# Kernel tuning notes

Measured on AMD Instinct MI355X. Metric: run time of the kernel, lower is better.

Reference implementation:

```python
import jax, jax.numpy as jnp
import numpy as np
import math

STRIDES = [8, 16, 32, 64, 128]
NUM_CLASSES = 80
NUM_ANCHORS = 9
_RATIOS = np.array([0.5, 1.0, 2.0])
_SCALES = 2.0 ** np.array([0.0, 1.0 / 3.0, 2.0 / 3.0])


def _base_anchors(base_size):
    # standard RetinaNet base anchors: 3 ratios x 3 scales, centered at origin
    a = np.zeros((9, 4))
    a[:, 2:] = base_size * np.tile(_SCALES, (2, 3)).T
    areas = a[:, 2] * a[:, 3]
    a[:, 2] = np.sqrt(areas / np.repeat(_RATIOS, 3))
    a[:, 3] = a[:, 2] * np.repeat(_RATIOS, 3)
    a[:, 0::2] -= np.tile(a[:, 2] * 0.5, (2, 1)).T
    a[:, 1::2] -= np.tile(a[:, 3] * 0.5, (2, 1)).T
    return a


def _make_anchors(featmap_sizes):
    per_level = []
    for (h, w), s in zip(featmap_sizes, STRIDES):
        base = _base_anchors(4 * s)  # base_size = 4 * stride (RetinaNet convention)
        sx = (np.arange(w) + 0.5) * s
        sy = (np.arange(h) + 0.5) * s
        X, Y = np.meshgrid(sx, sy)
        shifts = np.stack([X.ravel(), Y.ravel(), X.ravel(), Y.ravel()], axis=1)
        # anchors vary fastest per location -> matches [B,H,W,A,*] flatten order
        per_level.append((shifts[:, None, :] + base[None, :, :]).reshape(-1, 4))
    return jnp.asarray(np.concatenate(per_level, axis=0), dtype=jnp.float32)


def _conv3x3(x, w, b):
    y = jax.lax.conv_general_dilated(x, w, (1, 1), 'SAME', dimension_numbers=('NCHW', 'OIHW', 'NCHW'))
    return y + b[None, :, None, None]


def _tower(x, ws, bs):
    for i in range(4):
        x = jax.nn.relu(_conv3x3(x, ws[i], bs[i]))
    return _conv3x3(x, ws[4], bs[4])


def _bbox_transform(anchors, deltas):
    # BBoxTransform with mean 0, std (0.1, 0.1, 0.2, 0.2)
    w = anchors[:, 2] - anchors[:, 0]
    h = anchors[:, 3] - anchors[:, 1]
    cx = anchors[:, 0] + 0.5 * w
    cy = anchors[:, 1] + 0.5 * h
    pcx = cx + deltas[..., 0] * 0.1 * w
    pcy = cy + deltas[..., 1] * 0.1 * h
    pw = jnp.exp(deltas[..., 2] * 0.2) * w
    ph = jnp.exp(deltas[..., 3] * 0.2) * h
    return jnp.stack([pcx - 0.5 * pw, pcy - 0.5 * ph, pcx + 0.5 * pw, pcy + 0.5 * ph], axis=-1)


def _heads(feats, cls_ws, cls_bs, reg_ws, reg_bs):
    B = feats[0].shape[0]
    cls_l, reg_l = [], []
    for f in feats:
        c = _tower(f, cls_ws, cls_bs)  # [B, 9*80, H, W]
        cls_l.append(jnp.transpose(c, (0, 2, 3, 1)).reshape(B, -1, NUM_CLASSES))
        r = _tower(f, reg_ws, reg_bs)  # [B, 9*4, H, W]
        reg_l.append(jnp.transpose(r, (0, 2, 3, 1)).reshape(B, -1, 4))
    return jnp.concatenate(cls_l, axis=1), jnp.concatenate(reg_l, axis=1)


def setup_inputs():
    key = jax.random.key(0)
    ks = jax.random.split(key, 32)
    B, C = 8, 256
    sizes = [(64, 64), (32, 32), (16, 16), (8, 8), (4, 4)]
    inp = {}
    for i, (h, w) in enumerate(sizes):
        inp['feat%d' % i] = jax.random.normal(ks[i], (B, C, h, w), dtype=jnp.float32)
    prior_bias = -math.log((1.0 - 0.01) / 0.01)

    def mk(k, out_ch, in_ch):
        std = math.sqrt(2.0 / (9.0 * out_ch))  # matches torch init normal_(0, sqrt(2/n))
        return jax.random.normal(k, (out_ch, in_ch, 3, 3), dtype=jnp.float32) * std

    ki = 5
    for i in range(4):
        inp['cls_w%d' % i] = mk(ks[ki], 256, 256); ki += 1
        inp['cls_b%d' % i] = jnp.zeros((256,), jnp.float32)
    inp['cls_w4'] = mk(ks[ki], NUM_ANCHORS * NUM_CLASSES, 256); ki += 1
    inp['cls_b4'] = jnp.full((NUM_ANCHORS * NUM_CLASSES,), prior_bias, jnp.float32)
    for i in range(4):
        inp['reg_w%d' % i] = mk(ks[ki], 256, 256); ki += 1
        inp['reg_b%d' % i] = jnp.zeros((256,), jnp.float32)
    inp['reg_w4'] = mk(ks[ki], NUM_ANCHORS * 4, 256); ki += 1
    inp['reg_b4'] = jnp.full((NUM_ANCHORS * 4,), prior_bias, jnp.float32)
    return inp


def reference(feat0, feat1, feat2, feat3, feat4,
              cls_w0, cls_b0, cls_w1, cls_b1, cls_w2, cls_b2, cls_w3, cls_b3, cls_w4, cls_b4,
              reg_w0, reg_b0, reg_w1, reg_b1, reg_w2, reg_b2, reg_w3, reg_b3, reg_w4, reg_b4):
    feats = [feat0, feat1, feat2, feat3, feat4]
    cls_ws = [cls_w0, cls_w1, cls_w2, cls_w3, cls_w4]
    cls_bs = [cls_b0, cls_b1, cls_b2, cls_b3, cls_b4]
    reg_ws = [reg_w0, reg_w1, reg_w2, reg_w3, reg_w4]
    reg_bs = [reg_b0, reg_b1, reg_b2, reg_b3, reg_b4]
    pred_cls, pred_reg = _heads(feats, cls_ws, cls_bs, reg_ws, reg_bs)
    anchors = _make_anchors([f.shape[-2:] for f in feats])  # [A, 4]
    boxes = _bbox_transform(anchors, pred_reg)  # [B, A, 4]
    probs = jax.nn.sigmoid(pred_cls)  # [B, A, 80]
    scores = jnp.max(probs, axis=2)
    class_id = jnp.argmax(probs, axis=2)
    return scores, class_id, boxes
```

## Files before the change

kernel.cpp:

```cpp
#include <hip/hip_runtime.h>
#include <math.h>

#define CIN 256
#define TLW 16
#define TLH 8
#define LIS 22

template<typename TI, typename TA, int CH, bool RELU>
__global__ __launch_bounds__(256, 2) void conv_tile(
    const TI* __restrict__ in, const float* __restrict__ wgt,
    const float* __restrict__ bias, TA* __restrict__ out,
    int H, int W, int C_out)
{
    const int NCH = CIN / CH;
    const int tilesX = (W + TLW - 1) / TLW;
    const int tx = (blockIdx.x % tilesX) * TLW;
    const int ty = (blockIdx.x / tilesX) * TLH;
    const int b  = blockIdx.y;
    const int co0 = blockIdx.z * 64;
    const int tid = threadIdx.x;
    const int tco = (tid >> 5) * 8;
    const int tpx = tid & 31;
    const int prow = tpx >> 2;
    const int pcol = (tpx & 3) * 4;

    __shared__ __align__(16) TA lw[CH * 9 * 64];
    __shared__ __align__(16) TA li[CH * 10 * LIS];

    TA acc[8][4];
    #pragma unroll
    for (int c = 0; c < 8; ++c)
        #pragma unroll
        for (int j = 0; j < 4; ++j) acc[c][j] = (TA)0;

    const int coLim = min(64, C_out - co0);

    for (int ch = 0; ch < NCH; ++ch) {
        const int ci0 = ch * CH;
        for (int idx = tid; idx < CH * 9 * 64; idx += 256) {
            int r  = idx >> 6;
            int co = idx & 63;
            TA v = (TA)0;
            if (co < coLim)
                v = (TA)wgt[(size_t)(co0 + co) * (CIN * 9) + (size_t)ci0 * 9 + r];
            lw[idx] = v;
        }
        for (int idx = tid; idx < CH * 10 * LIS; idx += 256) {
            int ci = idx / (10 * LIS);
            int rr = idx % (10 * LIS);
            int row = rr / LIS, col = rr % LIS;
            TA v = (TA)0;
            int iy = ty + row - 1, ix = tx + col - 1;
            if (col < TLW + 2 && iy >= 0 && iy < H && ix >= 0 && ix < W)
                v = (TA)in[(((size_t)b * CIN + ci0 + ci) * H + iy) * W + ix];
            li[idx] = v;
        }
        __syncthreads();
        #pragma unroll
        for (int ci = 0; ci < CH; ++ci) {
            #pragma unroll
            for (int ky = 0; ky < 3; ++ky) {
                const TA* ip = &li[ci * 10 * LIS + (prow + ky) * LIS + pcol];
                TA ir[6];
                #pragma unroll
                for (int t = 0; t < 6; ++t) ir[t] = ip[t];
                #pragma unroll
                for (int kx = 0; kx < 3; ++kx) {
                    const TA* wp = &lw[(ci * 9 + ky * 3 + kx) * 64 + tco];
                    TA wv[8];
                    #pragma unroll
                    for (int c = 0; c < 8; ++c) wv[c] = wp[c];
                    TA x0 = ir[kx], x1 = ir[kx + 1], x2 = ir[kx + 2], x3 = ir[kx + 3];
                    #pragma unroll
                    for (int c = 0; c < 8; ++c) {
                        acc[c][0] += wv[c] * x0;
                        acc[c][1] += wv[c] * x1;
                        acc[c][2] += wv[c] * x2;
                        acc[c][3] += wv[c] * x3;
                    }
                }
            }
        }
        __syncthreads();
    }

    const int oy = ty + prow;
    if (oy < H) {
        #pragma unroll
        for (int c = 0; c < 8; ++c) {
            int co = co0 + tco + c;
            if (co < C_out) {
                TA bv = (TA)bias[co];
                #pragma unroll
                for (int j = 0; j < 4; ++j) {
                    int ox = tx + pcol + j;
                    if (ox < W) {
                        TA v = acc[c][j] + bv;
                        if (RELU) v = v > (TA)0 ? v : (TA)0;
                        out[(((size_t)b * C_out + co) * H + oy) * W + ox] = v;
                    }
                }
            }
        }
    }
}

#define CH5 8
__global__ __launch_bounds__(256, 2) void conv_cls5(
    const double* __restrict__ in, const float* __restrict__ wgt,
    const float* __restrict__ bias, float* __restrict__ scores,
    float* __restrict__ cls_id,
    int H, int W, int level_off, int A_total, int b0)
{
    const int tilesX = (W + TLW - 1) / TLW;
    const int tx = (blockIdx.x % tilesX) * TLW;
    const int ty = (blockIdx.x / tilesX) * TLH;
    const int b  = blockIdx.y;
    const int a  = blockIdx.z;
    const int co0 = a * 80;
    const int tid = threadIdx.x;
    const int cog = tid >> 5;
    const int tco = cog * 10;
    const int tpx = tid & 31;
    const int prow = tpx >> 2;
    const int pcol = (tpx & 3) * 4;

    __shared__ __align__(16) double lw[CH5 * 9 * 80];
    __shared__ __align__(16) double li[CH5 * 10 * LIS];

    double acc[10][4];
    #pragma unroll
    for (int c = 0; c < 10; ++c)
        #pragma unroll
        for (int j = 0; j < 4; ++j) acc[c][j] = 0.0;

    for (int ch = 0; ch < CIN / CH5; ++ch) {
        const int ci0 = ch * CH5;
        for (int idx = tid; idx < CH5 * 9 * 80; idx += 256) {
            int r  = idx / 80;
            int co = idx % 80;
            lw[idx] = (double)wgt[(size_t)(co0 + co) * (CIN * 9)
                                  + (size_t)ci0 * 9 + r];
        }
        for (int idx = tid; idx < CH5 * 10 * LIS; idx += 256) {
            int ci = idx / (10 * LIS);
            int rr = idx % (10 * LIS);
            int row = rr / LIS, col = rr % LIS;
            double v = 0.0;
            int iy = ty + row - 1, ix = tx + col - 1;
            if (col < TLW + 2 && iy >= 0 && iy < H && ix >= 0 && ix < W)
                v = in[(((size_t)b * CIN + ci0 + ci) * H + iy) * W + ix];
            li[idx] = v;
        }
        __syncthreads();
        #pragma unroll
        for (int ci = 0; ci < CH5; ++ci) {
            #pragma unroll
            for (int ky = 0; ky < 3; ++ky) {
                const double* ip = &li[ci * 10 * LIS + (prow + ky) * LIS + pcol];
                double ir[6];
                #pragma unroll
                for (int t = 0; t < 6; ++t) ir[t] = ip[t];
                #pragma unroll
                for (int kx = 0; kx < 3; ++kx) {
                    const double* wp = &lw[(ci * 9 + ky * 3 + kx) * 80 + tco];
                    double wv[10];
                    #pragma unroll
                    for (int c = 0; c < 10; ++c) wv[c] = wp[c];
                    double x0 = ir[kx], x1 = ir[kx + 1], x2 = ir[kx + 2], x3 = ir[kx + 3];
                    #pragma unroll
                    for (int c = 0; c < 10; ++c) {
                        acc[c][0] += wv[c] * x0;
                        acc[c][1] += wv[c] * x1;
                        acc[c][2] += wv[c] * x2;
                        acc[c][3] += wv[c] * x3;
                    }
                }
            }
        }
        __syncthreads();
    }

    double* redM = lw;
    int*    redA = (int*)li;

    #pragma unroll
    for (int j = 0; j < 4; ++j) {
        double m = acc[0][j] + (double)bias[co0 + tco];
        int am = tco;
        #pragma unroll
        for (int c = 1; c < 10; ++c) {
            double v = acc[c][j] + (double)bias[co0 + tco + c];
            if (v > m) { m = v; am = tco + c; }
        }
        int p = prow * 16 + pcol + j;
        redM[p * 8 + cog] = m;
        redA[p * 8 + cog] = am;
    }
    __syncthreads();
    if (tid < 128) {
        int p = tid;
        double m = redM[p * 8]; int am = redA[p * 8];
        #pragma unroll
        for (int t = 1; t < 8; ++t)
            if (redM[p * 8 + t] > m) { m = redM[p * 8 + t]; am = redA[p * 8 + t]; }
        int oy = ty + (p >> 4), ox = tx + (p & 15);
        if (oy < H && ox < W) {
            size_t oi = (size_t)(b0 + b) * A_total + level_off
                      + (size_t)(oy * W + ox) * 9 + a;
            scores[oi] = (float)(1.0 / (1.0 + exp(-m)));
            cls_id[oi] = (float)am;
        }
    }
}

__global__ void boxes_ep(const float* __restrict__ reg5, float* __restrict__ boxes,
                         int H, int W, int level_off, int A_total, float stride,
                         int b0, int Bc)
{
    int idx = blockIdx.x * 256 + threadIdx.x;
    int total = Bc * H * W * 9;
    if (idx >= total) return;
    int a = idx % 9; int rest = idx / 9;
    int x = rest % W; rest /= W;
    int y = rest % H; int b = rest / H;

    float base = 4.f * stride;
    float scale = exp2f((float)(a % 3) * (1.f / 3.f));
    int ri = a / 3;
    float sr = (ri == 0) ? 0.70710678118654752f : (ri == 1 ? 1.f : 1.41421356237309505f);
    float wa = base * scale / sr;
    float ha = base * scale * sr;
    float cx = (x + 0.5f) * stride, cy = (y + 0.5f) * stride;

    size_t cs = (size_t)H * W;
    const float* rp = reg5 + (((size_t)b * 36 + a * 4) * H + y) * W + x;
    float d0 = rp[0], d1 = rp[cs], d2 = rp[2 * cs], d3 = rp[3 * cs];

    float pcx = cx + d0 * 0.1f * wa;
    float pcy = cy + d1 * 0.1f * ha;
    float pw  = expf(d2 * 0.2f) * wa;
    float ph  = expf(d3 * 0.2f) * ha;

    size_t oi = ((size_t)(b0 + b) * A_total + level_off
               + (size_t)(y * W + x) * 9 + a) * 4;
    boxes[oi + 0] = pcx - 0.5f * pw;
    boxes[oi + 1] = pcy - 0.5f * ph;
    boxes[oi + 2] = pcx + 0.5f * pw;
    boxes[oi + 3] = pcy + 0.5f * ph;
}

extern "C" void kernel_launch(void* const* d_in, const int* in_sizes, int n_in,
                              void* d_out, int out_size, void* d_ws, size_t ws_size,
                              hipStream_t stream)
{
    const float* feats[5];
    for (int i = 0; i < 5; ++i) feats[i] = (const float*)d_in[i];
    const float* cw[5]; const float* cb[5];
    const float* rw[5]; const float* rb[5];
    for (int i = 0; i < 5; ++i) {
        cw[i] = (const float*)d_in[5 + 2 * i];
        cb[i] = (const float*)d_in[6 + 2 * i];
        rw[i] = (const float*)d_in[15 + 2 * i];
        rb[i] = (const float*)d_in[16 + 2 * i];
    }

    const int A_total = 49104;
    float* scores = (float*)d_out;
    float* cls_id = scores + (size_t)8 * A_total;
    float* boxes  = scores + (size_t)2 * 8 * A_total;

    const int   Hs[5]      = {64, 32, 16, 8, 4};
    const float strides[5] = {8.f, 16.f, 32.f, 64.f, 128.f};
    const int   offs[5]    = {0, 36864, 46080, 48384, 48960};

    for (int l = 0; l < 5; ++l) {
        int H = Hs[l], W = Hs[l];
        size_t perb = (size_t)CIN * H * W;
        int Bc = 8;
        while (Bc > 1 && 2ull * Bc * perb * sizeof(double) > ws_size) Bc >>= 1;
        double* D0 = (double*)d_ws;
        double* D1 = D0 + (size_t)Bc * perb;
        int tiles = ((W + TLW - 1) / TLW) * ((H + TLH - 1) / TLH);
        for (int b0 = 0; b0 < 8; b0 += Bc) {
            dim3 g(tiles, Bc, 4);
            const float* fin = feats[l] + (size_t)b0 * perb;
            conv_tile<float,  double, 8, true><<<g, 256, 0, stream>>>(fin, cw[0], cb[0], D0, H, W, 256);
            conv_tile<double, double, 8, true><<<g, 256, 0, stream>>>(D0,  cw[1], cb[1], D1, H, W, 256);
            conv_tile<double, double, 8, true><<<g, 256, 0, stream>>>(D1,  cw[2], cb[2], D0, H, W, 256);
            conv_tile<double, double, 8, true><<<g, 256, 0, stream>>>(D0,  cw[3], cb[3], D1, H, W, 256);
            dim3 g5(tiles, Bc, 9);
            conv_cls5<<<g5, 256, 0, stream>>>(D1, cw[4], cb[4], scores, cls_id,
                                              H, W, offs[l], A_total, b0);
        }
    }

    for (int l = 0; l < 5; ++l) {
        int H = Hs[l], W = Hs[l];
        size_t perb = (size_t)CIN * H * W;
        int Br = 8;
        while (Br > 1 && 2ull * Br * perb * sizeof(float) > ws_size) Br >>= 1;
        float* F0 = (float*)d_ws;
        float* F1 = F0 + (size_t)Br * perb;
        int tiles = ((W + TLW - 1) / TLW) * ((H + TLH - 1) / TLH);
        for (int b0 = 0; b0 < 8; b0 += Br) {
            dim3 g(tiles, Br, 4);
            const float* fin = feats[l] + (size_t)b0 * perb;
            conv_tile<float, float, 8, true><<<g, 256, 0, stream>>>(fin, rw[0], rb[0], F0, H, W, 256);
            conv_tile<float, float, 8, true><<<g, 256, 0, stream>>>(F0,  rw[1], rb[1], F1, H, W, 256);
            conv_tile<float, float, 8, true><<<g, 256, 0, stream>>>(F1,  rw[2], rb[2], F0, H, W, 256);
            conv_tile<float, float, 8, true><<<g, 256, 0, stream>>>(F0,  rw[3], rb[3], F1, H, W, 256);
            dim3 gr(tiles, Br, 1);
            conv_tile<float, float, 8, false><<<gr, 256, 0, stream>>>(F1, rw[4], rb[4], F0, H, W, 36);
            int total = Br * H * W * 9;
            boxes_ep<<<(total + 255) / 256, 256, 0, stream>>>(F0, boxes, H, W,
                                                              offs[l], A_total,
                                                              strides[l], b0, Br);
        }
    }
}
```

Measured before the change: 25.01 ms.

## Pre-transpose weights and read them as wave-uniform scalar loads instead of LDS

```diff
diff --git a/kernel.cpp b/kernel.cpp
--- a/kernel.cpp
+++ b/kernel.cpp
@@ -2,81 +2,104 @@
 #include <math.h>
 
 #define CIN 256
+#define K9  2304
 #define TLW 16
 #define TLH 8
 #define LIS 22
 
-template<typename TI, typename TA, int CH, bool RELU>
-__global__ __launch_bounds__(256, 2) void conv_tile(
-    const TI* __restrict__ in, const float* __restrict__ wgt,
+__global__ void cvt_w(const float* __restrict__ cw0, const float* __restrict__ cw1,
+                      const float* __restrict__ cw2, const float* __restrict__ cw3,
+                      const float* __restrict__ cw4,
+                      const float* __restrict__ rw0, const float* __restrict__ rw1,
+                      const float* __restrict__ rw2, const float* __restrict__ rw3,
+                      const float* __restrict__ rw4,
+                      double* __restrict__ W64, double* __restrict__ W64_5,
+                      float* __restrict__ W32, float* __restrict__ W32_5)
+{
+    int idx = blockIdx.x * 256 + threadIdx.x;
+    const int N1 = 4 * K9 * 256, N2 = K9 * 720, N3 = 4 * K9 * 256, N4 = K9 * 36;
+    if (idx < N1) {
+        int l = idx / (K9 * 256); int rem = idx % (K9 * 256);
+        int r = rem / 256, co = rem % 256;
+        const float* s = l == 0 ? cw0 : l == 1 ? cw1 : l == 2 ? cw2 : cw3;
+        W64[idx] = (double)s[(size_t)co * K9 + r];
+        return;
+    }
+    idx -= N1;
+    if (idx < N2) {
+        int r = idx / 720, co = idx % 720;
+        W64_5[idx] = (double)cw4[(size_t)co * K9 + r];
+        return;
+    }
+    idx -= N2;
+    if (idx < N3) {
+        int l = idx / (K9 * 256); int rem = idx % (K9 * 256);
+        int r = rem / 256, co = rem % 256;
+        const float* s = l == 0 ? rw0 : l == 1 ? rw1 : l == 2 ? rw2 : rw3;
+        W32[idx] = s[(size_t)co * K9 + r];
+        return;
+    }
+    idx -= N3;
+    if (idx < N4) {
+        int r = idx / 36, co = idx % 36;
+        W32_5[idx] = rw4[(size_t)co * K9 + r];
+    }
+}
+
+template<typename TI, typename TA, int CH, int CO_W, bool RELU>
+__global__ __launch_bounds__(256, 3) void conv_s(
+    const TI* __restrict__ in, const TA* __restrict__ wgtT,
     const float* __restrict__ bias, TA* __restrict__ out,
-    int H, int W, int C_out)
+    int H, int W, int CO_TOT)
 {
     const int NCH = CIN / CH;
     const int tilesX = (W + TLW - 1) / TLW;
     const int tx = (blockIdx.x % tilesX) * TLW;
     const int ty = (blockIdx.x / tilesX) * TLH;
     const int b  = blockIdx.y;
-    const int co0 = blockIdx.z * 64;
     const int tid = threadIdx.x;
-    const int tco = (tid >> 5) * 8;
-    const int tpx = tid & 31;
-    const int prow = tpx >> 2;
-    const int pcol = (tpx & 3) * 4;
-
-    __shared__ __align__(16) TA lw[CH * 9 * 64];
+    const int w  = __builtin_amdgcn_readfirstlane(tid >> 6);
+    const int lane = tid & 63;
+    const int row = lane >> 3;
+    const int c2  = (lane & 7) * 2;
+    const int co_base = blockIdx.z * (4 * CO_W) + w * CO_W;
+
     __shared__ __align__(16) TA li[CH * 10 * LIS];
 
-    TA acc[8][4];
+    TA acc[CO_W][2];
     #pragma unroll
-    for (int c = 0; c < 8; ++c)
-        #pragma unroll
-        for (int j = 0; j < 4; ++j) acc[c][j] = (TA)0;
-
-    const int coLim = min(64, C_out - co0);
+    for (int c = 0; c < CO_W; ++c) { acc[c][0] = (TA)0; acc[c][1] = (TA)0; }
 
     for (int ch = 0; ch < NCH; ++ch) {
         const int ci0 = ch * CH;
-        for (int idx = tid; idx < CH * 9 * 64; idx += 256) {
-            int r  = idx >> 6;
-            int co = idx & 63;
-            TA v = (TA)0;
-            if (co < coLim)
-                v = (TA)wgt[(size_t)(co0 + co) * (CIN * 9) + (size_t)ci0 * 9 + r];
-            lw[idx] = v;
-        }
         for (int idx = tid; idx < CH * 10 * LIS; idx += 256) {
             int ci = idx / (10 * LIS);
             int rr = idx % (10 * LIS);
-            int row = rr / LIS, col = rr % LIS;
+            int r = rr / LIS, col = rr % LIS;
             TA v = (TA)0;
-            int iy = ty + row - 1, ix = tx + col - 1;
+            int iy = ty + r - 1, ix = tx + col - 1;
             if (col < TLW + 2 && iy >= 0 && iy < H && ix >= 0 && ix < W)
                 v = (TA)in[(((size_t)b * CIN + ci0 + ci) * H + iy) * W + ix];
             li[idx] = v;
         }
         __syncthreads();
-        #pragma unroll
+        #pragma unroll 4
         for (int ci = 0; ci < CH; ++ci) {
             #pragma unroll
             for (int ky = 0; ky < 3; ++ky) {
-                const TA* ip = &li[ci * 10 * LIS + (prow + ky) * LIS + pcol];
-                TA ir[6];
-                #pragma unroll
-                for (int t = 0; t < 6; ++t) ir[t] = ip[t];
+                const TA* ip = &li[(ci * 10 + row + ky) * LIS + c2];
+                TA ir0 = ip[0], ir1 = ip[1], ir2 = ip[2], ir3 = ip[3];
                 #pragma unroll
                 for (int kx = 0; kx < 3; ++kx) {
-                    const TA* wp = &lw[(ci * 9 + ky * 3 + kx) * 64 + tco];
-                    TA wv[8];
+                    const int r = (ci0 + ci) * 9 + ky * 3 + kx;
+                    const TA* wp = wgtT + (size_t)r * CO_TOT + co_base;
+                    TA x0 = (kx == 0) ? ir0 : (kx == 1) ? ir1 : ir2;
+                    TA x1 = (kx == 0) ? ir1 : (kx == 1) ? ir2 : ir3;
                     #pragma unroll
-                    for (int c = 0; c < 8; ++c) wv[c] = wp[c];
-                    TA x0 = ir[kx], x1 = ir[kx + 1], x2 = ir[kx + 2], x3 = ir[kx + 3];
-                    #pragma unroll
-                    for (int c = 0; c < 8; ++c) {
-                        acc[c][0] += wv[c] * x0;
-                        acc[c][1] += wv[c] * x1;
-                        acc[c][2] += wv[c] * x2;
-                        acc[c][3] += wv[c] * x3;
+                    for (int c = 0; c < CO_W; ++c) {
+                        TA wv = wp[c];
+                        acc[c][0] += wv * x0;
+                        acc[c][1] += wv * x1;
                     }
                 }
             }
@@ -84,30 +107,26 @@
         __syncthreads();
     }
 
-    const int oy = ty + prow;
+    const int oy = ty + row;
+    const int ox = tx + c2;
     if (oy < H) {
         #pragma unroll
-        for (int c = 0; c < 8; ++c) {
-            int co = co0 + tco + c;
-            if (co < C_out) {
-                TA bv = (TA)bias[co];
-                #pragma unroll
-                for (int j = 0; j < 4; ++j) {
-                    int ox = tx + pcol + j;
-                    if (ox < W) {
-                        TA v = acc[c][j] + bv;
-                        if (RELU) v = v > (TA)0 ? v : (TA)0;
-                        out[(((size_t)b * C_out + co) * H + oy) * W + ox] = v;
-                    }
-                }
-            }
-        }
-    }
-}
-
-#define CH5 8
-__global__ __launch_bounds__(256, 2) void conv_cls5(
-    const double* __restrict__ in, const float* __restrict__ wgt,
+        for (int c = 0; c < CO_W; ++c) {
+            int co = co_base + c;
+            TA bv = (TA)bias[co];
+            TA v0 = acc[c][0] + bv;
+            TA v1 = acc[c][1] + bv;
+            if (RELU) { v0 = v0 > (TA)0 ? v0 : (TA)0; v1 = v1 > (TA)0 ? v1 : (TA)0; }
+            size_t o = (((size_t)b * CO_TOT + co) * H + oy) * W + ox;
+            if (ox + 1 < W) { out[o] = v0; out[o + 1] = v1; }
+            else if (ox < W) { out[o] = v0; }
+        }
+    }
+}
+
+#define CH5 16
+__global__ __launch_bounds__(256, 3) void conv_cls5s(
+    const double* __restrict__ in, const double* __restrict__ wgtT,
     const float* __restrict__ bias, float* __restrict__ scores,
     float* __restrict__ cls_id,
     int H, int W, int level_off, int A_total, int b0)
@@ -117,63 +136,52 @@
     const int ty = (blockIdx.x / tilesX) * TLH;
     const int b  = blockIdx.y;
     const int a  = blockIdx.z;
-    const int co0 = a * 80;
     const int tid = threadIdx.x;
-    const int cog = tid >> 5;
-    const int tco = cog * 10;
-    const int tpx = tid & 31;
-    const int prow = tpx >> 2;
-    const int pcol = (tpx & 3) * 4;
-
-    __shared__ __align__(16) double lw[CH5 * 9 * 80];
+    const int w  = __builtin_amdgcn_readfirstlane(tid >> 6);
+    const int lane = tid & 63;
+    const int row = lane >> 3;
+    const int c2  = (lane & 7) * 2;
+    const int co_loc  = w * 20;
+    const int co_base = a * 80 + co_loc;
+
     __shared__ __align__(16) double li[CH5 * 10 * LIS];
-
-    double acc[10][4];
+    __shared__ double redM[4][128];
+    __shared__ int    redA[4][128];
+
+    double acc[20][2];
     #pragma unroll
-    for (int c = 0; c < 10; ++c)
-        #pragma unroll
-        for (int j = 0; j < 4; ++j) acc[c][j] = 0.0;
+    for (int c = 0; c < 20; ++c) { acc[c][0] = 0.0; acc[c][1] = 0.0; }
 
     for (int ch = 0; ch < CIN / CH5; ++ch) {
         const int ci0 = ch * CH5;
-        for (int idx = tid; idx < CH5 * 9 * 80; idx += 256) {
-            int r  = idx / 80;
-            int co = idx % 80;
-            lw[idx] = (double)wgt[(size_t)(co0 + co) * (CIN * 9)
-                                  + (size_t)ci0 * 9 + r];
-        }
         for (int idx = tid; idx < CH5 * 10 * LIS; idx += 256) {
             int ci = idx / (10 * LIS);
             int rr = idx % (10 * LIS);
-            int row = rr / LIS, col = rr % LIS;
+            int r = rr / LIS, col = rr % LIS;
             double v = 0.0;
-            int iy = ty + row - 1, ix = tx + col - 1;
+            int iy = ty + r - 1, ix = tx + col - 1;
             if (col < TLW + 2 && iy >= 0 && iy < H && ix >= 0 && ix < W)
                 v = in[(((size_t)b * CIN + ci0 + ci) * H + iy) * W + ix];
             li[idx] = v;
         }
         __syncthreads();
-        #pragma unroll
+        #pragma unroll 2
         for (int ci = 0; ci < CH5; ++ci) {
             #pragma unroll
             for (int ky = 0; ky < 3; ++ky) {
-                const double* ip = &li[ci * 10 * LIS + (prow + ky) * LIS + pcol];
-                double ir[6];
-                #pragma unroll
-                for (int t = 0; t < 6; ++t) ir[t] = ip[t];
+                const double* ip = &li[(ci * 10 + row + ky) * LIS + c2];
+                double ir0 = ip[0], ir1 = ip[1], ir2 = ip[2], ir3 = ip[3];
                 #pragma unroll
                 for (int kx = 0; kx < 3; ++kx) {
-                    const double* wp = &lw[(ci * 9 + ky * 3 + kx) * 80 + tco];
-                    double wv[10];
+                    const int r = (ci0 + ci) * 9 + ky * 3 + kx;
+                    const double* wp = wgtT + (size_t)r * 720 + co_base;
+                    double x0 = (kx == 0) ? ir0 : (kx == 1) ? ir1 : ir2;
+                    double x1 = (kx == 0) ? ir1 : (kx == 1) ? ir2 : ir3;
                     #pragma unroll
-                    for (int c = 0; c < 10; ++c) wv[c] = wp[c];
-                    double x0 = ir[kx], x1 = ir[kx + 1], x2 = ir[kx + 2], x3 = ir[kx + 3];
-                    #pragma unroll
-                    for (int c = 0; c < 10; ++c) {
-                        acc[c][0] += wv[c] * x0;
-                        acc[c][1] += wv[c] * x1;
-                        acc[c][2] += wv[c] * x2;
-                        acc[c][3] += wv[c] * x3;
+                    for (int c = 0; c < 20; ++c) {
+                        double wv = wp[c];
+                        acc[c][0] += wv * x0;
+                        acc[c][1] += wv * x1;
                     }
                 }
             }
@@ -181,29 +189,26 @@
         __syncthreads();
     }
 
-    double* redM = lw;
-    int*    redA = (int*)li;
-
     #pragma unroll
-    for (int j = 0; j < 4; ++j) {
-        double m = acc[0][j] + (double)bias[co0 + tco];
-        int am = tco;
+    for (int j = 0; j < 2; ++j) {
+        double m = acc[0][j] + (double)bias[a * 80 + co_loc];
+        int am = co_loc;
         #pragma unroll
-        for (int c = 1; c < 10; ++c) {
-            double v = acc[c][j] + (double)bias[co0 + tco + c];
-            if (v > m) { m = v; am = tco + c; }
-        }
-        int p = prow * 16 + pcol + j;
-        redM[p * 8 + cog] = m;
-        redA[p * 8 + cog] = am;
+        for (int c = 1; c < 20; ++c) {
+            double v = acc[c][j] + (double)bias[a * 80 + co_loc + c];
+            if (v > m) { m = v; am = co_loc + c; }
+        }
+        int p = row * 16 + c2 + j;
+        redM[w][p] = m;
+        redA[w][p] = am;
     }
     __syncthreads();
     if (tid < 128) {
         int p = tid;
-        double m = redM[p * 8]; int am = redA[p * 8];
+        double m = redM[0][p]; int am = redA[0][p];
         #pragma unroll
-        for (int t = 1; t < 8; ++t)
-            if (redM[p * 8 + t] > m) { m = redM[p * 8 + t]; am = redA[p * 8 + t]; }
+        for (int t = 1; t < 4; ++t)
+            if (redM[t][p] > m) { m = redM[t][p]; am = redA[t][p]; }
         int oy = ty + (p >> 4), ox = tx + (p & 15);
         if (oy < H && ox < W) {
             size_t oi = (size_t)(b0 + b) * A_total + level_off
@@ -274,24 +279,50 @@
     const float strides[5] = {8.f, 16.f, 32.f, 64.f, 128.f};
     const int   offs[5]    = {0, 36864, 46080, 48384, 48960};
 
+    const size_t S1 = (size_t)4 * K9 * 256 * 8;
+    const size_t S2 = (size_t)K9 * 720 * 8;
+    const size_t S3 = (size_t)4 * K9 * 256 * 4;
+    const size_t S4 = (size_t)K9 * 36 * 4 + 256;
+    char* p = (char*)d_ws;
+    double* W64   = (double*)p;            p += S1;
+    double* W64_5 = (double*)p;            p += S2;
+    float*  W32   = (float*)p;             p += S3;
+    float*  W32_5 = (float*)p;             p += S4;
+    size_t wsW = (size_t)(p - (char*)d_ws);
+    wsW = (wsW + 255) & ~(size_t)255;
+    char*  actBase  = (char*)d_ws + wsW;
+    size_t actBytes = ws_size > wsW ? ws_size - wsW : 0;
+
+    {
+        int Ntot = 4 * K9 * 256 + K9 * 720 + 4 * K9 * 256 + K9 * 36;
+        cvt_w<<<(Ntot + 255) / 256, 256, 0, stream>>>(
+            cw[0], cw[1], cw[2], cw[3], cw[4],
+            rw[0], rw[1], rw[2], rw[3], rw[4],
+            W64, W64_5, W32, W32_5);
+    }
+
     for (int l = 0; l < 5; ++l) {
         int H = Hs[l], W = Hs[l];
         size_t perb = (size_t)CIN * H * W;
         int Bc = 8;
-        while (Bc > 1 && 2ull * Bc * perb * sizeof(double) > ws_size) Bc >>= 1;
-        double* D0 = (double*)d_ws;
+        while (Bc > 1 && 2ull * Bc * perb * 8 > actBytes) Bc >>= 1;
+        double* D0 = (double*)actBase;
         double* D1 = D0 + (size_t)Bc * perb;
         int tiles = ((W + TLW - 1) / TLW) * ((H + TLH - 1) / TLH);
         for (int b0 = 0; b0 < 8; b0 += Bc) {
             dim3 g(tiles, Bc, 4);
             const float* fin = feats[l] + (size_t)b0 * perb;
-            conv_tile<float,  double, 8, true><<<g, 256, 0, stream>>>(fin, cw[0], cb[0], D0, H, W, 256);
-            conv_tile<double, double, 8, true><<<g, 256, 0, stream>>>(D0,  cw[1], cb[1], D1, H, W, 256);
-            conv_tile<double, double, 8, true><<<g, 256, 0, stream>>>(D1,  cw[2], cb[2], D0, H, W, 256);
-            conv_tile<double, double, 8, true><<<g, 256, 0, stream>>>(D0,  cw[3], cb[3], D1, H, W, 256);
+            conv_s<float,  double, 16, 16, true><<<g, 256, 0, stream>>>(
+                fin, W64 + 0 * (size_t)K9 * 256, cb[0], D0, H, W, 256);
+            conv_s<double, double, 16, 16, true><<<g, 256, 0, stream>>>(
+                D0,  W64 + 1 * (size_t)K9 * 256, cb[1], D1, H, W, 256);
+            conv_s<double, double, 16, 16, true><<<g, 256, 0, stream>>>(
+                D1,  W64 + 2 * (size_t)K9 * 256, cb[2], D0, H, W, 256);
+            conv_s<double, double, 16, 16, true><<<g, 256, 0, stream>>>(
+                D0,  W64 + 3 * (size_t)K9 * 256, cb[3], D1, H, W, 256);
             dim3 g5(tiles, Bc, 9);
-            conv_cls5<<<g5, 256, 0, stream>>>(D1, cw[4], cb[4], scores, cls_id,
-                                              H, W, offs[l], A_total, b0);
+            conv_cls5s<<<g5, 256, 0, stream>>>(D1, W64_5, cb[4], scores, cls_id,
+                                               H, W, offs[l], A_total, b0);
         }
     }
 
@@ -299,19 +330,24 @@
         int H = Hs[l], W = Hs[l];
         size_t perb = (size_t)CIN * H * W;
         int Br = 8;
-        while (Br > 1 && 2ull * Br * perb * sizeof(float) > ws_size) Br >>= 1;
-        float* F0 = (float*)d_ws;
+        while (Br > 1 && 2ull * Br * perb * 4 > actBytes) Br >>= 1;
+        float* F0 = (float*)actBase;
         float* F1 = F0 + (size_t)Br * perb;
         int tiles = ((W + TLW - 1) / TLW) * ((H + TLH - 1) / TLH);
         for (int b0 = 0; b0 < 8; b0 += Br) {
             dim3 g(tiles, Br, 4);
             const float* fin = feats[l] + (size_t)b0 * perb;
-            conv_tile<float, float, 8, true><<<g, 256, 0, stream>>>(fin, rw[0], rb[0], F0, H, W, 256);
-            conv_tile<float, float, 8, true><<<g, 256, 0, stream>>>(F0,  rw[1], rb[1], F1, H, W, 256);
-            conv_tile<float, float, 8, true><<<g, 256, 0, stream>>>(F1,  rw[2], rb[2], F0, H, W, 256);
-            conv_tile<float, float, 8, true><<<g, 256, 0, stream>>>(F0,  rw[3], rb[3], F1, H, W, 256);
+            conv_s<float, float, 16, 16, true><<<g, 256, 0, stream>>>(
+                fin, W32 + 0 * (size_t)K9 * 256, rb[0], F0, H, W, 256);
+            conv_s<float, float, 16, 16, true><<<g, 256, 0, stream>>>(
+                F0,  W32 + 1 * (size_t)K9 * 256, rb[1], F1, H, W, 256);
+            conv_s<float, float, 16, 16, true><<<g, 256, 0, stream>>>(
+                F1,  W32 + 2 * (size_t)K9 * 256, rb[2], F0, H, W, 256);
+            conv_s<float, float, 16, 16, true><<<g, 256, 0, stream>>>(
+                F0,  W32 + 3 * (size_t)K9 * 256, rb[3], F1, H, W, 256);
             dim3 gr(tiles, Br, 1);
-            conv_tile<float, float, 8, false><<<gr, 256, 0, stream>>>(F1, rw[4], rb[4], F0, H, W, 36);
+            conv_s<float, float, 16, 9, false><<<gr, 256, 0, stream>>>(
+                F1, W32_5, rb[4], F0, H, W, 36);
             int total = Br * H * W * 9;
             boxes_ep<<<(total + 255) / 256, 256, 0, stream>>>(F0, boxes, H, W,
                                                               offs[l], A_total,
```

After: 33.49 ms. 33.9% more time.

## Use FP64 MFMA for classification tower convolutions with pre-transposed double weights

Applied to the files above, without the earlier changes.

```diff
diff --git a/kernel.cpp b/kernel.cpp
--- a/kernel.cpp
+++ b/kernel.cpp
@@ -2,9 +2,256 @@
 #include <math.h>
 
 #define CIN 256
+#define K9  2304
 #define TLW 16
 #define TLH 8
 #define LIS 22
+
+typedef double f64x4 __attribute__((ext_vector_type(4)));
+typedef double f64x2 __attribute__((ext_vector_type(2)));
+
+#if defined(__has_builtin)
+#  if __has_builtin(__builtin_amdgcn_mfma_f64_16x16x4f64)
+#    define MFMA64(A,B,C) __builtin_amdgcn_mfma_f64_16x16x4f64((A),(B),(C),0,0,0)
+#    define HAVE_MFMA64 1
+#  elif __has_builtin(__builtin_amdgcn_mfma_f64_16x16x4_f64)
+#    define MFMA64(A,B,C) __builtin_amdgcn_mfma_f64_16x16x4_f64((A),(B),(C),0,0,0)
+#    define HAVE_MFMA64 1
+#  endif
+#endif
+#ifndef HAVE_MFMA64
+#  define HAVE_MFMA64 0
+#  define MFMA64(A,B,C) (C)
+#endif
+
+__global__ void cvt_w64(const float* __restrict__ cw0, const float* __restrict__ cw1,
+                        const float* __restrict__ cw2, const float* __restrict__ cw3,
+                        const float* __restrict__ cw4,
+                        double* __restrict__ W64, double* __restrict__ W64_5)
+{
+    int idx = blockIdx.x * 256 + threadIdx.x;
+    const int N1 = 4 * K9 * 256, N2 = K9 * 720;
+    if (idx < N1) {
+        int l = idx / (K9 * 256); int rem = idx % (K9 * 256);
+        int r = rem / 256, co = rem % 256;
+        const float* s = l == 0 ? cw0 : l == 1 ? cw1 : l == 2 ? cw2 : cw3;
+        W64[idx] = (double)s[(size_t)co * K9 + r];
+        return;
+    }
+    idx -= N1;
+    if (idx < N2) {
+        int r = idx / 720, co = idx % 720;
+        W64_5[idx] = (double)cw4[(size_t)co * K9 + r];
+    }
+}
+
+template<typename TI, bool RELU>
+__global__ __launch_bounds__(256) void conv_m64(
+    const TI* __restrict__ in, const double* __restrict__ wgtT,
+    const float* __restrict__ bias, double* __restrict__ out,
+    int H, int W)
+{
+    const int tilesX = (W + 15) >> 4;
+    const int tx = (blockIdx.x % tilesX) * 16;
+    const int ty = (blockIdx.x / tilesX) * 16;
+    const int b  = blockIdx.y;
+    const int co0 = blockIdx.z * 64;
+    const int tid = threadIdx.x;
+    const int w   = tid >> 6;
+    const int lane = tid & 63;
+    const int l15 = lane & 15;
+    const int lq  = lane >> 4;
+
+    __shared__ __align__(16) double li[8 * 18 * 20];
+    __shared__ __align__(16) double lb[4 * 9 * 64 * 2];
+
+    const f64x4 zero4 = {0.0, 0.0, 0.0, 0.0};
+    f64x4 acc[4][4];
+    #pragma unroll
+    for (int mt = 0; mt < 4; ++mt)
+        #pragma unroll
+        for (int nt = 0; nt < 4; ++nt) acc[mt][nt] = zero4;
+
+    int laneAoff[18];
+    #pragma unroll
+    for (int s = 0; s < 18; ++s) {
+        int k = s * 4 + lq;
+        int ci = k / 9, tap = k % 9;
+        laneAoff[s] = (ci * 18 + tap / 3) * 20 + tap % 3;
+    }
+    int mtOff[4];
+    #pragma unroll
+    for (int mt = 0; mt < 4; ++mt) mtOff[mt] = (w * 4 + mt) * 20 + l15;
+
+    for (int ch = 0; ch < 32; ++ch) {
+        const int ci0 = ch * 8;
+        for (int idx = tid; idx < 8 * 18 * 20; idx += 256) {
+            int ci = idx / 360;
+            int rr = idx % 360;
+            int row = rr / 20, col = rr % 20;
+            double v = 0.0;
+            int iy = ty + row - 1, ix = tx + col - 1;
+            if (col < 18 && iy >= 0 && iy < H && ix >= 0 && ix < W)
+                v = (double)in[(((size_t)b * CIN + ci0 + ci) * H + iy) * W + ix];
+            li[idx] = v;
+        }
+        for (int idx = tid; idx < 72 * 64; idx += 256) {
+            int k = idx >> 6, co = idx & 63;
+            int kq = k & 3, k4 = k >> 2;
+            lb[((kq * 9 + (k4 >> 1)) * 64 + co) * 2 + (k4 & 1)] =
+                wgtT[(size_t)(ci0 * 9 + k) * 256 + co0 + co];
+        }
+        __syncthreads();
+        #pragma unroll
+        for (int kp = 0; kp < 9; ++kp) {
+            f64x2 bf[4];
+            #pragma unroll
+            for (int nt = 0; nt < 4; ++nt)
+                bf[nt] = *(const f64x2*)&lb[((lq * 9 + kp) * 64 + nt * 16 + l15) * 2];
+            #pragma unroll
+            for (int mt = 0; mt < 4; ++mt) {
+                double a0 = li[laneAoff[2 * kp]     + mtOff[mt]];
+                double a1 = li[laneAoff[2 * kp + 1] + mtOff[mt]];
+                #pragma unroll
+                for (int nt = 0; nt < 4; ++nt) {
+                    acc[mt][nt] = MFMA64(a0, bf[nt][0], acc[mt][nt]);
+                    acc[mt][nt] = MFMA64(a1, bf[nt][1], acc[mt][nt]);
+                }
+            }
+        }
+        __syncthreads();
+    }
+
+    #pragma unroll
+    for (int mt = 0; mt < 4; ++mt) {
+        int oy = ty + w * 4 + mt;
+        if (oy >= H) continue;
+        #pragma unroll
+        for (int nt = 0; nt < 4; ++nt) {
+            int co = co0 + nt * 16 + l15;
+            double bv = (double)bias[co];
+            #pragma unroll
+            for (int j = 0; j < 4; ++j) {
+                int ox = tx + lq * 4 + j;
+                if (ox < W) {
+                    double v = acc[mt][nt][j] + bv;
+                    if (RELU) v = v > 0.0 ? v : 0.0;
+                    out[(((size_t)b * 256 + co) * H + oy) * W + ox] = v;
+                }
+            }
+        }
+    }
+}
+
+__global__ __launch_bounds__(256) void cls5_m64(
+    const double* __restrict__ in, const double* __restrict__ wgtT5,
+    const float* __restrict__ bias, float* __restrict__ scores,
+    float* __restrict__ cls_id,
+    int H, int W, int level_off, int A_total, int b0)
+{
+    const int tilesX = (W + 15) >> 4;
+    const int tx = (blockIdx.x % tilesX) * 16;
+    const int ty = (blockIdx.x / tilesX) * 8;
+    const int b  = blockIdx.y;
+    const int a  = blockIdx.z;
+    const int tid = threadIdx.x;
+    const int w   = tid >> 6;
+    const int lane = tid & 63;
+    const int l15 = lane & 15;
+    const int lq  = lane >> 4;
+
+    __shared__ __align__(16) double li[8 * 10 * 20];
+    __shared__ __align__(16) double lb[4 * 9 * 80 * 2];
+
+    const f64x4 zero4 = {0.0, 0.0, 0.0, 0.0};
+    f64x4 acc[2][5];
+    #pragma unroll
+    for (int mt = 0; mt < 2; ++mt)
+        #pragma unroll
+        for (int nt = 0; nt < 5; ++nt) acc[mt][nt] = zero4;
+
+    int laneAoff[18];
+    #pragma unroll
+    for (int s = 0; s < 18; ++s) {
+        int k = s * 4 + lq;
+        int ci = k / 9, tap = k % 9;
+        laneAoff[s] = (ci * 10 + tap / 3) * 20 + tap % 3;
+    }
+    int mtOff[2];
+    #pragma unroll
+    for (int mt = 0; mt < 2; ++mt) mtOff[mt] = (w * 2 + mt) * 20 + l15;
+
+    for (int ch = 0; ch < 32; ++ch) {
+        const int ci0 = ch * 8;
+        for (int idx = tid; idx < 8 * 10 * 20; idx += 256) {
+            int ci = idx / 200;
+            int rr = idx % 200;
+            int row = rr / 20, col = rr % 20;
+            double v = 0.0;
+            int iy = ty + row - 1, ix = tx + col - 1;
+            if (col < 18 && iy >= 0 && iy < H && ix >= 0 && ix < W)
+                v = in[(((size_t)b * CIN + ci0 + ci) * H + iy) * W + ix];
+            li[idx] = v;
+        }
+        for (int idx = tid; idx < 72 * 80; idx += 256) {
+            int k = idx / 80, co = idx % 80;
+            int kq = k & 3, k4 = k >> 2;
+            lb[((kq * 9 + (k4 >> 1)) * 80 + co) * 2 + (k4 & 1)] =
+                wgtT5[(size_t)(ci0 * 9 + k) * 720 + a * 80 + co];
+        }
+        __syncthreads();
+        #pragma unroll
+        for (int kp = 0; kp < 9; ++kp) {
+            f64x2 bf[5];
+            #pragma unroll
+            for (int nt = 0; nt < 5; ++nt)
+                bf[nt] = *(const f64x2*)&lb[((lq * 9 + kp) * 80 + nt * 16 + l15) * 2];
+            #pragma unroll
+            for (int mt = 0; mt < 2; ++mt) {
+                double a0 = li[laneAoff[2 * kp]     + mtOff[mt]];
+                double a1 = li[laneAoff[2 * kp + 1] + mtOff[mt]];
+                #pragma unroll
+                for (int nt = 0; nt < 5; ++nt) {
+                    acc[mt][nt] = MFMA64(a0, bf[nt][0], acc[mt][nt]);
+                    acc[mt][nt] = MFMA64(a1, bf[nt][1], acc[mt][nt]);
+                }
+            }
+        }
+        __syncthreads();
+    }
+
+    double bv[5];
+    #pragma unroll
+    for (int nt = 0; nt < 5; ++nt) bv[nt] = (double)bias[a * 80 + nt * 16 + l15];
+
+    #pragma unroll
+    for (int mt = 0; mt < 2; ++mt) {
+        int oy = ty + w * 2 + mt;
+        #pragma unroll
+        for (int j = 0; j < 4; ++j) {
+            double m = acc[mt][0][j] + bv[0];
+            int am = l15;
+            #pragma unroll
+            for (int nt = 1; nt < 5; ++nt) {
+                double v = acc[mt][nt][j] + bv[nt];
+                if (v > m) { m = v; am = nt * 16 + l15; }
+            }
+            #pragma unroll
+            for (int mask = 1; mask < 16; mask <<= 1) {
+                double m2 = __shfl_xor(m, mask);
+                int am2 = __shfl_xor(am, mask);
+                if (m2 > m || (m2 == m && am2 < am)) { m = m2; am = am2; }
+            }
+            int ox = tx + lq * 4 + j;
+            if (l15 == 0 && oy < H && ox < W) {
+                size_t oi = (size_t)(b0 + b) * A_total + level_off
+                          + (size_t)(oy * W + ox) * 9 + a;
+                scores[oi] = (float)(1.0 / (1.0 + exp(-m)));
+                cls_id[oi] = (float)am;
+            }
+        }
+    }
+}
 
 template<typename TI, typename TA, int CH, bool RELU>
 __global__ __launch_bounds__(256, 2) void conv_tile(
@@ -274,24 +521,57 @@
     const float strides[5] = {8.f, 16.f, 32.f, 64.f, 128.f};
     const int   offs[5]    = {0, 36864, 46080, 48384, 48960};
 
+    const size_t S1 = (size_t)4 * K9 * 256 * 8;
+    const size_t S2 = (size_t)K9 * 720 * 8;
+    char* p = (char*)d_ws;
+    double* W64   = (double*)p;            p += S1;
+    double* W64_5 = (double*)p;            p += S2;
+    size_t wsW = (size_t)(p - (char*)d_ws);
+    wsW = (wsW + 255) & ~(size_t)255;
+    char*  actBase  = (char*)d_ws + wsW;
+    size_t actBytes = ws_size > wsW ? ws_size - wsW : 0;
+
+    if (HAVE_MFMA64) {
+        int Ntot = 4 * K9 * 256 + K9 * 720;
+        cvt_w64<<<(Ntot + 255) / 256, 256, 0, stream>>>(
+            cw[0], cw[1], cw[2], cw[3], cw[4], W64, W64_5);
+    }
+
     for (int l = 0; l < 5; ++l) {
         int H = Hs[l], W = Hs[l];
         size_t perb = (size_t)CIN * H * W;
         int Bc = 8;
-        while (Bc > 1 && 2ull * Bc * perb * sizeof(double) > ws_size) Bc >>= 1;
-        double* D0 = (double*)d_ws;
+        while (Bc > 1 && 2ull * Bc * perb * 8 > actBytes) Bc >>= 1;
+        double* D0 = (double*)actBase;
         double* D1 = D0 + (size_t)Bc * perb;
-        int tiles = ((W + TLW - 1) / TLW) * ((H + TLH - 1) / TLH);
         for (int b0 = 0; b0 < 8; b0 += Bc) {
-            dim3 g(tiles, Bc, 4);
             const float* fin = feats[l] + (size_t)b0 * perb;
-            conv_tile<float,  double, 8, true><<<g, 256, 0, stream>>>(fin, cw[0], cb[0], D0, H, W, 256);
-            conv_tile<double, double, 8, true><<<g, 256, 0, stream>>>(D0,  cw[1], cb[1], D1, H, W, 256);
-            conv_tile<double, double, 8, true><<<g, 256, 0, stream>>>(D1,  cw[2], cb[2], D0, H, W, 256);
-            conv_tile<double, double, 8, true><<<g, 256, 0, stream>>>(D0,  cw[3], cb[3], D1, H, W, 256);
-            dim3 g5(tiles, Bc, 9);
-            conv_cls5<<<g5, 256, 0, stream>>>(D1, cw[4], cb[4], scores, cls_id,
-                                              H, W, offs[l], A_total, b0);
+            if (HAVE_MFMA64) {
+                int tiles16 = ((W + 15) / 16) * ((H + 15) / 16);
+                int tiles5  = ((W + 15) / 16) * ((H + 7) / 8);
+                dim3 g(tiles16, Bc, 4);
+                conv_m64<float,  true><<<g, 256, 0, stream>>>(
+                    fin, W64 + 0 * (size_t)K9 * 256, cb[0], D0, H, W);
+                conv_m64<double, true><<<g, 256, 0, stream>>>(
+                    D0,  W64 + 1 * (size_t)K9 * 256, cb[1], D1, H, W);
+                conv_m64<double, true><<<g, 256, 0, stream>>>(
+                    D1,  W64 + 2 * (size_t)K9 * 256, cb[2], D0, H, W);
+                conv_m64<double, true><<<g, 256, 0, stream>>>(
+                    D0,  W64 + 3 * (size_t)K9 * 256, cb[3], D1, H, W);
+                dim3 g5(tiles5, Bc, 9);
+                cls5_m64<<<g5, 256, 0, stream>>>(D1, W64_5, cb[4], scores, cls_id,
+                                                 H, W, offs[l], A_total, b0);
+            } else {
+                int tiles = ((W + TLW - 1) / TLW) * ((H + TLH - 1) / TLH);
+                dim3 g(tiles, Bc, 4);
+                conv_tile<float,  double, 8, true><<<g, 256, 0, stream>>>(fin, cw[0], cb[0], D0, H, W, 256);
+                conv_tile<double, double, 8, true><<<g, 256, 0, stream>>>(D0,  cw[1], cb[1], D1, H, W, 256);
+                conv_tile<double, double, 8, true><<<g, 256, 0, stream>>>(D1,  cw[2], cb[2], D0, H, W, 256);
+                conv_tile<double, double, 8, true><<<g, 256, 0, stream>>>(D0,  cw[3], cb[3], D1, H, W, 256);
+                dim3 g5(tiles, Bc, 9);
+                conv_cls5<<<g5, 256, 0, stream>>>(D1, cw[4], cb[4], scores, cls_id,
+                                                  H, W, offs[l], A_total, b0);
+            }
         }
     }
 
@@ -299,8 +579,8 @@
         int H = Hs[l], W = Hs[l];
         size_t perb = (size_t)CIN * H * W;
         int Br = 8;
-        while (Br > 1 && 2ull * Br * perb * sizeof(float) > ws_size) Br >>= 1;
-        float* F0 = (float*)d_ws;
+        while (Br > 1 && 2ull * Br * perb * 4 > actBytes) Br >>= 1;
+        float* F0 = (float*)actBase;
         float* F1 = F0 + (size_t)Br * perb;
         int tiles = ((W + TLW - 1) / TLW) * ((H + TLH - 1) / TLH);
         for (int b0 = 0; b0 < 8; b0 += Br) {
```

Result: no change. 25.04 ms (+0.1%).

## Compute final cls conv in fp32 with fp64 fixup for near-tie argmax

Applied to the files above, without the earlier changes.

```diff
diff --git a/kernel.cpp b/kernel.cpp
--- a/kernel.cpp
+++ b/kernel.cpp
@@ -2,9 +2,11 @@
 #include <math.h>
 
 #define CIN 256
+#define K9  2304
 #define TLW 16
 #define TLH 8
 #define LIS 22
+#define TAU 1e-3f
 
 template<typename TI, typename TA, int CH, bool RELU>
 __global__ __launch_bounds__(256, 2) void conv_tile(
@@ -106,10 +108,10 @@
 }
 
 #define CH5 8
-__global__ __launch_bounds__(256, 2) void conv_cls5(
+__global__ __launch_bounds__(256, 2) void cls5_f32(
     const double* __restrict__ in, const float* __restrict__ wgt,
     const float* __restrict__ bias, float* __restrict__ scores,
-    float* __restrict__ cls_id,
+    float* __restrict__ cls_id, unsigned char* __restrict__ flags,
     int H, int W, int level_off, int A_total, int b0)
 {
     const int tilesX = (W + TLW - 1) / TLW;
@@ -125,31 +127,33 @@
     const int prow = tpx >> 2;
     const int pcol = (tpx & 3) * 4;
 
-    __shared__ __align__(16) double lw[CH5 * 9 * 80];
-    __shared__ __align__(16) double li[CH5 * 10 * LIS];
-
-    double acc[10][4];
+    __shared__ __align__(16) float lw[CH5 * 9 * 80];
+    __shared__ __align__(16) float li[CH5 * 10 * LIS];
+    __shared__ float redM1[128 * 8];
+    __shared__ float redM2[128 * 8];
+    __shared__ int   redA [128 * 8];
+
+    float acc[10][4];
     #pragma unroll
     for (int c = 0; c < 10; ++c)
         #pragma unroll
-        for (int j = 0; j < 4; ++j) acc[c][j] = 0.0;
+        for (int j = 0; j < 4; ++j) acc[c][j] = 0.f;
 
     for (int ch = 0; ch < CIN / CH5; ++ch) {
         const int ci0 = ch * CH5;
         for (int idx = tid; idx < CH5 * 9 * 80; idx += 256) {
             int r  = idx / 80;
             int co = idx % 80;
-            lw[idx] = (double)wgt[(size_t)(co0 + co) * (CIN * 9)
-                                  + (size_t)ci0 * 9 + r];
+            lw[idx] = wgt[(size_t)(co0 + co) * (CIN * 9) + (size_t)ci0 * 9 + r];
         }
         for (int idx = tid; idx < CH5 * 10 * LIS; idx += 256) {
             int ci = idx / (10 * LIS);
             int rr = idx % (10 * LIS);
             int row = rr / LIS, col = rr % LIS;
-            double v = 0.0;
+            float v = 0.f;
             int iy = ty + row - 1, ix = tx + col - 1;
             if (col < TLW + 2 && iy >= 0 && iy < H && ix >= 0 && ix < W)
-                v = in[(((size_t)b * CIN + ci0 + ci) * H + iy) * W + ix];
+                v = (float)in[(((size_t)b * CIN + ci0 + ci) * H + iy) * W + ix];
             li[idx] = v;
         }
         __syncthreads();
@@ -157,23 +161,23 @@
         for (int ci = 0; ci < CH5; ++ci) {
             #pragma unroll
             for (int ky = 0; ky < 3; ++ky) {
-                const double* ip = &li[ci * 10 * LIS + (prow + ky) * LIS + pcol];
-                double ir[6];
+                const float* ip = &li[ci * 10 * LIS + (prow + ky) * LIS + pcol];
+                float ir[6];
                 #pragma unroll
                 for (int t = 0; t < 6; ++t) ir[t] = ip[t];
                 #pragma unroll
                 for (int kx = 0; kx < 3; ++kx) {
-                    const double* wp = &lw[(ci * 9 + ky * 3 + kx) * 80 + tco];
-                    double wv[10];
+                    const float* wp = &lw[(ci * 9 + ky * 3 + kx) * 80 + tco];
+                    float wv[10];
                     #pragma unroll
                     for (int c = 0; c < 10; ++c) wv[c] = wp[c];
-                    double x0 = ir[kx], x1 = ir[kx + 1], x2 = ir[kx + 2], x3 = ir[kx + 3];
+                    float x0 = ir[kx], x1 = ir[kx + 1], x2 = ir[kx + 2], x3 = ir[kx + 3];
                     #pragma unroll
                     for (int c = 0; c < 10; ++c) {
-                        acc[c][0] += wv[c] * x0;
-                        acc[c][1] += wv[c] * x1;
-                        acc[c][2] += wv[c] * x2;
-                        acc[c][3] += wv[c] * x3;
+                        acc[c][0] = fmaf(wv[c], x0, acc[c][0]);
+                        acc[c][1] = fmaf(wv[c], x1, acc[c][1]);
+                        acc[c][2] = fmaf(wv[c], x2, acc[c][2]);
+                        acc[c][3] = fmaf(wv[c], x3, acc[c][3]);
                     }
                 }
             }
@@ -181,33 +185,83 @@
         __syncthreads();
     }
 
-    double* redM = lw;
-    int*    redA = (int*)li;
-
     #pragma unroll
     for (int j = 0; j < 4; ++j) {
-        double m = acc[0][j] + (double)bias[co0 + tco];
+        float m1 = acc[0][j] + bias[co0 + tco];
+        float m2 = -3.0e38f;
         int am = tco;
         #pragma unroll
         for (int c = 1; c < 10; ++c) {
-            double v = acc[c][j] + (double)bias[co0 + tco + c];
-            if (v > m) { m = v; am = tco + c; }
+            float v = acc[c][j] + bias[co0 + tco + c];
+            if (v > m1) { m2 = m1; m1 = v; am = tco + c; }
+            else if (v > m2) { m2 = v; }
         }
         int p = prow * 16 + pcol + j;
-        redM[p * 8 + cog] = m;
-        redA[p * 8 + cog] = am;
+        redM1[p * 8 + cog] = m1;
+        redA [p * 8 + cog] = am;
+        redM2[p * 8 + cog] = m2;
     }
     __syncthreads();
     if (tid < 128) {
         int p = tid;
-        double m = redM[p * 8]; int am = redA[p * 8];
-        #pragma unroll
-        for (int t = 1; t < 8; ++t)
-            if (redM[p * 8 + t] > m) { m = redM[p * 8 + t]; am = redA[p * 8 + t]; }
+        float m1 = redM1[p * 8]; int am = redA[p * 8]; float m2 = redM2[p * 8];
+        #pragma unroll
+        for (int t = 1; t < 8; ++t) {
+            float rm1 = redM1[p * 8 + t];
+            float rm2 = redM2[p * 8 + t];
+            if (rm1 > m1) { m2 = fmaxf(m1, rm2); m1 = rm1; am = redA[p * 8 + t]; }
+            else          { m2 = fmaxf(m2, rm1); }
+        }
         int oy = ty + (p >> 4), ox = tx + (p & 15);
         if (oy < H && ox < W) {
             size_t oi = (size_t)(b0 + b) * A_total + level_off
                       + (size_t)(oy * W + ox) * 9 + a;
+            scores[oi] = 1.f / (1.f + expf(-m1));
+            cls_id[oi] = (float)am;
+            flags[((size_t)b * H * W + oy * W + ox) * 9 + a] =
+                (m1 - m2 < TAU) ? 1 : 0;
+        }
+    }
+}
+
+__global__ __launch_bounds__(128) void fixup_cls(
+    const double* __restrict__ in, const float* __restrict__ wgt,
+    const float* __restrict__ bias, const unsigned char* __restrict__ flags,
+    float* __restrict__ scores, float* __restrict__ cls_id,
+    int H, int W, int level_off, int A_total, int b0)
+{
+    const int px = blockIdx.x;
+    const int b  = blockIdx.y;
+    const int a  = blockIdx.z;
+    const int tid = threadIdx.x;
+    const unsigned char fl = flags[((size_t)b * H * W + px) * 9 + a];
+
+    __shared__ double patch[K9];
+    __shared__ double lg[80];
+
+    if (fl) {
+        const int y = px / W, x = px % W;
+        for (int idx = tid; idx < K9; idx += 128) {
+            int ci = idx / 9, tap = idx % 9;
+            int iy = y + tap / 3 - 1, ix = x + tap % 3 - 1;
+            double v = 0.0;
+            if (iy >= 0 && iy < H && ix >= 0 && ix < W)
+                v = in[(((size_t)b * CIN + ci) * H + iy) * W + ix];
+            patch[idx] = v;
+        }
+        __syncthreads();
+        if (tid < 80) {
+            const float* wr = wgt + (size_t)(a * 80 + tid) * K9;
+            double s = 0.0;
+            for (int k = 0; k < K9; ++k) s += (double)wr[k] * patch[k];
+            lg[tid] = s + (double)bias[a * 80 + tid];
+        }
+        __syncthreads();
+        if (tid == 0) {
+            double m = lg[0]; int am = 0;
+            for (int c = 1; c < 80; ++c)
+                if (lg[c] > m) { m = lg[c]; am = c; }
+            size_t oi = (size_t)(b0 + b) * A_total + level_off + (size_t)px * 9 + a;
             scores[oi] = (float)(1.0 / (1.0 + exp(-m)));
             cls_id[oi] = (float)am;
         }
@@ -274,23 +328,32 @@
     const float strides[5] = {8.f, 16.f, 32.f, 64.f, 128.f};
     const int   offs[5]    = {0, 36864, 46080, 48384, 48960};
 
+    const size_t flagRes = 131072;
+    unsigned char* flags = (unsigned char*)d_ws;
+    char*  actBase  = (char*)d_ws + flagRes;
+    size_t actBytes = ws_size > flagRes ? ws_size - flagRes : 0;
+
     for (int l = 0; l < 5; ++l) {
         int H = Hs[l], W = Hs[l];
         size_t perb = (size_t)CIN * H * W;
         int Bc = 8;
-        while (Bc > 1 && 2ull * Bc * perb * sizeof(double) > ws_size) Bc >>= 1;
-        double* D0 = (double*)d_ws;
+        while (Bc > 1 && 2ull * Bc * perb * 8 > actBytes) Bc >>= 1;
+        double* D0 = (double*)actBase;
         double* D1 = D0 + (size_t)Bc * perb;
         int tiles = ((W + TLW - 1) / TLW) * ((H + TLH - 1) / TLH);
         for (int b0 = 0; b0 < 8; b0 += Bc) {
+            const float* fin = feats[l] + (size_t)b0 * perb;
             dim3 g(tiles, Bc, 4);
-            const float* fin = feats[l] + (size_t)b0 * perb;
             conv_tile<float,  double, 8, true><<<g, 256, 0, stream>>>(fin, cw[0], cb[0], D0, H, W, 256);
             conv_tile<double, double, 8, true><<<g, 256, 0, stream>>>(D0,  cw[1], cb[1], D1, H, W, 256);
             conv_tile<double, double, 8, true><<<g, 256, 0, stream>>>(D1,  cw[2], cb[2], D0, H, W, 256);
             conv_tile<double, double, 8, true><<<g, 256, 0, stream>>>(D0,  cw[3], cb[3], D1, H, W, 256);
             dim3 g5(tiles, Bc, 9);
-            conv_cls5<<<g5, 256, 0, stream>>>(D1, cw[4], cb[4], scores, cls_id,
+            cls5_f32<<<g5, 256, 0, stream>>>(D1, cw[4], cb[4], scores, cls_id,
+                                             flags, H, W, offs[l], A_total, b0);
+            dim3 gf(H * W, Bc, 9);
+            fixup_cls<<<gf, 128, 0, stream>>>(D1, cw[4], cb[4], flags,
+                                              scores, cls_id,
                                               H, W, offs[l], A_total, b0);
         }
     }
@@ -299,8 +362,8 @@
         int H = Hs[l], W = Hs[l];
         size_t perb = (size_t)CIN * H * W;
         int Br = 8;
-        while (Br > 1 && 2ull * Br * perb * sizeof(float) > ws_size) Br >>= 1;
-        float* F0 = (float*)d_ws;
+        while (Br > 1 && 2ull * Br * perb * 4 > actBytes) Br >>= 1;
+        float* F0 = (float*)actBase;
         float* F1 = F0 + (size_t)Br * perb;
         int tiles = ((W + TLW - 1) / TLW) * ((H + TLH - 1) / TLH);
         for (int b0 = 0; b0 < 8; b0 += Br) {
```

New measurement: 24.80 ms. Within noise of the previous version (-0.8%).
